# Kernel optimization log

Hardware: AMD Instinct MI355X
Metric: run time of the kernel (lower is better)

## Reference

```python
import jax, jax.numpy as jnp
import numpy as np

N = 100000          # nodes
E = 3200000         # edges (before self-loops)
F_IN = 500          # Pubmed feature dim
H1, C1 = 8, 8       # layer-1 heads, channels per head
H2, C2 = 1, 7       # layer-2 heads, channels (num classes)
NEG_SLOPE = 0.2


def _glorot(key, shape, fan_in):
    return jax.random.normal(key, shape, dtype=jnp.float32) / np.sqrt(fan_in)


def setup_inputs() -> dict:
    key = jax.random.key(0)
    ks = jax.random.split(key, 10)
    x = jax.random.normal(ks[0], (N, F_IN), dtype=jnp.float32)
    edge_index = jax.random.randint(ks[1], (2, E), 0, N, dtype=jnp.int64)
    W1 = _glorot(ks[2], (F_IN, H1 * C1), F_IN)
    a_src1 = _glorot(ks[3], (H1, C1), C1)
    a_dst1 = _glorot(ks[4], (H1, C1), C1)
    b1 = jnp.zeros((H1 * C1,), dtype=jnp.float32)
    W2 = _glorot(ks[5], (H1 * C1, H2 * C2), H1 * C1)
    a_src2 = _glorot(ks[6], (H2, C2), C2)
    a_dst2 = _glorot(ks[7], (H2, C2), C2)
    b2 = jnp.zeros((H2 * C2,), dtype=jnp.float32)
    return {"x": x, "edge_index": edge_index, "W1": W1, "a_src1": a_src1,
            "a_dst1": a_dst1, "b1": b1, "W2": W2, "a_src2": a_src2,
            "a_dst2": a_dst2, "b2": b2}


def gat_conv(x, src, dst, W, a_src, a_dst, bias, heads, out_ch):
    # x: [N, F_in]; src/dst: [E'] (self-loops included); returns [N, heads*out_ch]
    h = (x @ W).reshape(N, heads, out_ch)                      # [N, H, C]
    alpha_s = jnp.einsum('nhc,hc->nh', h, a_src)               # [N, H]
    alpha_d = jnp.einsum('nhc,hc->nh', h, a_dst)               # [N, H]
    e = alpha_s[src] + alpha_d[dst]                            # [E', H]
    e = jax.nn.leaky_relu(e, NEG_SLOPE)
    # segment softmax over incoming edges of each dst node
    m = jax.ops.segment_max(e, dst, num_segments=N)            # [N, H]
    ex = jnp.exp(e - m[dst])                                   # [E', H]
    denom = jax.ops.segment_sum(ex, dst, num_segments=N)       # [N, H]
    alpha = ex / denom[dst]                                    # [E', H]
    msg = alpha[:, :, None] * h[src]                           # [E', H, C]
    out = jax.ops.segment_sum(msg, dst, num_segments=N)        # [N, H, C]
    return out.reshape(N, heads * out_ch) + bias


def reference(x, edge_index, W1, a_src1, a_dst1, b1, W2, a_src2, a_dst2, b2):
    loops = jnp.arange(N, dtype=edge_index.dtype)
    src = jnp.concatenate([edge_index[0], loops])
    dst = jnp.concatenate([edge_index[1], loops])
    h = gat_conv(x, src, dst, W1, a_src1, a_dst1, b1, H1, C1)   # [N, 64]
    out = gat_conv(h, src, dst, W2, a_src2, a_dst2, b2, H2, C2) # [N, 7]
    return jax.nn.log_softmax(out, axis=1)
```

## Files before the change

### kernel.cpp

```cpp
#include <hip/hip_runtime.h>
#include <hip/hip_bf16.h>
#include <hip/hip_fp16.h>

#define N_NODES 100000
#define N_EDGES 3200000
#define ET (N_EDGES + N_NODES)
#define F_IN 500
#define H1 8
#define C1 8
#define F1 64
#define C2 7

#define BSH 6
#define NB ((N_NODES + 63) / 64)
#define CAP2 4096
#define FB 128
#define FCHUNK ((ET + FB - 1) / FB)

typedef __attribute__((ext_vector_type(8))) short short8;
typedef __attribute__((ext_vector_type(4))) float f32x4;

__device__ __forceinline__ unsigned short f2bf(float f) {
    const unsigned u = __float_as_uint(f);
    return (unsigned short)((u + 0x7FFFu + ((u >> 16) & 1u)) >> 16);
}

__global__ __launch_bounds__(1024) void fill_count(const int* __restrict__ ei,
                                                   int* __restrict__ cntmat) {
    __shared__ int hist[NB];
    const int t = threadIdx.x, blk = blockIdx.x;
    for (int i = t; i < NB; i += 1024) hist[i] = 0;
    __syncthreads();
    const int s0 = blk * FCHUNK;
    const int s1 = min(s0 + FCHUNK, ET);
    for (int i = s0 + t; i < s1; i += 1024) {
        const int dst = (i < N_EDGES) ? ei[N_EDGES + i] : (i - N_EDGES);
        atomicAdd(&hist[dst >> BSH], 1);
    }
    __syncthreads();
    int* row = cntmat + (size_t)blk * NB;
    for (int i = t; i < NB; i += 1024) row[i] = hist[i];
}

__global__ __launch_bounds__(1024) void scan2(const int* __restrict__ cntmat,
                                              int* __restrict__ boff,
                                              int* __restrict__ basemat) {
    __shared__ int tot[2048];
    __shared__ int wsum[16];
    const int t = threadIdx.x;
    const int lane = t & 63;
    const int w = t >> 6;
    for (int b = t; b < 2048; b += 1024) {
        int s = 0;
        if (b < NB)
            for (int j = 0; j < FB; ++j) s += cntmat[(size_t)j * NB + b];
        tot[b] = s;
    }
    __syncthreads();
    int running = 0;
    for (int t0 = 0; t0 < 2048; t0 += 1024) {
        const int v = tot[t0 + t];
        int sc = v;
#pragma unroll
        for (int d = 1; d < 64; d <<= 1) {
            int u = __shfl_up(sc, d);
            if (lane >= d) sc += u;
        }
        if (lane == 63) wsum[w] = sc;
        __syncthreads();
        if (t < 16) {
            int ws = wsum[t];
#pragma unroll
            for (int d = 1; d < 16; d <<= 1) {
                int u = __shfl_up(ws, d);
                if (t >= d) ws += u;
            }
            wsum[t] = ws;
        }
        __syncthreads();
        const int excl = running + (w ? wsum[w - 1] : 0) + sc - v;
        if (t0 + t < NB) boff[t0 + t] = excl;
        const int tt = wsum[15];
        __syncthreads();
        tot[t0 + t] = excl;
        running += tt;
    }
    if (t == 0) boff[NB] = running;
    __syncthreads();
    for (int b = t; b < NB; b += 1024) {
        int run = tot[b];
        for (int j = 0; j < FB; ++j) {
            basemat[(size_t)j * NB + b] = run;
            run += cntmat[(size_t)j * NB + b];
        }
    }
}

__global__ __launch_bounds__(1024) void fill_scatter(const int* __restrict__ ei,
                                                     const int* __restrict__ basemat,
                                                     unsigned int* __restrict__ ebuf) {
    __shared__ int cur[NB];
    const int t = threadIdx.x, blk = blockIdx.x;
    const int* row = basemat + (size_t)blk * NB;
    for (int i = t; i < NB; i += 1024) cur[i] = row[i];
    __syncthreads();
    const int s0 = blk * FCHUNK;
    const int s1 = min(s0 + FCHUNK, ET);
    for (int i = s0 + t; i < s1; i += 1024) {
        int src, dst;
        if (i < N_EDGES) { src = ei[i]; dst = ei[N_EDGES + i]; }
        else             { src = dst = i - N_EDGES; }
        const int b = dst >> BSH;
        const int p = atomicAdd(&cur[b], 1);
        ebuf[p] = (unsigned)src | ((unsigned)(dst & 63) << 17);
    }
}

__global__ __launch_bounds__(256) void wprep(const float* __restrict__ W1,
                                             short* __restrict__ wpk) {
    const int idx = blockIdx.x * 256 + threadIdx.x;
    if (idx >= 32768) return;
    const int j = idx & 7;
    const int l = (idx >> 3) & 63;
    const int f = (idx >> 9) & 3;
    const int ks = idx >> 11;
    const int k = ks * 32 + ((l >> 4) << 3) + j;
    const int col = f * 16 + (l & 15);
    const float fv = (k < F_IN) ? W1[k * F1 + col] : 0.f;
    wpk[idx] = (short)f2bf(fv);
}

__global__ __launch_bounds__(256) void gemm1_kernel(
    const float* __restrict__ x, const short* __restrict__ wpk,
    const float* __restrict__ a_src, const float* __restrict__ a_dst,
    __half* __restrict__ h1, float* __restrict__ as1, float* __restrict__ ad1)
{
    const int t = threadIdx.x;
    const int l = t & 63;
    const int w = t >> 6;
    const int row0 = blockIdx.x * 64 + w * 16;
    const int r = l & 15;
    const int koff = (l >> 4) * 8;
    const float* __restrict__ xp =
        x + (size_t)min(row0 + r, N_NODES - 1) * F_IN + koff;
    const short* __restrict__ wl = wpk + (l << 3);

    f32x4 acc[4];
#pragma unroll
    for (int f = 0; f < 4; ++f) acc[f] = (f32x4){0.f, 0.f, 0.f, 0.f};

    float4 va = *(const float4*)(xp);
    float4 vb = *(const float4*)(xp + 4);
    short8 bcur[4];
#pragma unroll
    for (int f = 0; f < 4; ++f)
        bcur[f] = *(const short8*)(wl + (f << 9));

    for (int ks = 0; ks < 16; ++ks) {
        float v[8];
        v[0] = va.x; v[1] = va.y; v[2] = va.z; v[3] = va.w;
        v[4] = vb.x; v[5] = vb.y; v[6] = vb.z; v[7] = vb.w;
        if (ks < 14) {
            va = *(const float4*)(xp + (ks + 1) * 32);
            vb = *(const float4*)(xp + (ks + 1) * 32 + 4);
        } else if (ks == 14) {
            float tv[8];
#pragma unroll
            for (int j = 0; j < 8; ++j)
                tv[j] = (koff + j < 20) ? xp[480 + j] : 0.f;
            va = make_float4(tv[0], tv[1], tv[2], tv[3]);
            vb = make_float4(tv[4], tv[5], tv[6], tv[7]);
        }
        short8 bnext[4];
        if (ks < 15) {
#pragma unroll
            for (int f = 0; f < 4; ++f)
                bnext[f] = *(const short8*)(wl + (((ks + 1) * 4 + f) << 9));
        }
        short8 ah, al;
#pragma unroll
        for (int j = 0; j < 8; ++j) {
            const unsigned short h = f2bf(v[j]);
            ah[j] = (short)h;
            al[j] = (short)f2bf(v[j] - __uint_as_float((unsigned)h << 16));
        }
#pragma unroll
        for (int f = 0; f < 4; ++f) {
            acc[f] = __builtin_amdgcn_mfma_f32_16x16x32_bf16(ah, bcur[f], acc[f], 0, 0, 0);
            acc[f] = __builtin_amdgcn_mfma_f32_16x16x32_bf16(al, bcur[f], acc[f], 0, 0, 0);
        }
        if (ks < 15) {
#pragma unroll
            for (int f = 0; f < 4; ++f) bcur[f] = bnext[f];
        }
    }

    const int g = l >> 4;
    const int p = r >> 3;
    float asv[4], adv[4];
#pragma unroll
    for (int f = 0; f < 4; ++f) {
        asv[f] = a_src[f * 16 + r];
        adv[f] = a_dst[f * 16 + r];
    }
#pragma unroll
    for (int f = 0; f < 4; ++f) {
#pragma unroll
        for (int reg = 0; reg < 4; ++reg) {
            const int row = row0 + g * 4 + reg;
            const float hv = acc[f][reg];
            if (row < N_NODES)
                h1[(size_t)row * F1 + f * 16 + r] = __float2half(hv);
            float ps = hv * asv[f];
            float pd = hv * adv[f];
            ps += __shfl_xor(ps, 1); ps += __shfl_xor(ps, 2); ps += __shfl_xor(ps, 4);
            pd += __shfl_xor(pd, 1); pd += __shfl_xor(pd, 2); pd += __shfl_xor(pd, 4);
            if ((l & 7) == 0 && row < N_NODES) {
                as1[row * H1 + f * 2 + p] = ps;
                ad1[row * H1 + f * 2 + p] = pd;
            }
        }
    }
}

__global__ __launch_bounds__(256) void agg1_kernel(
    const int* __restrict__ boff, const unsigned int* __restrict__ ebuf,
    const __half* __restrict__ h1, const float* __restrict__ as1,
    const float* __restrict__ ad1, const float* __restrict__ b1,
    float* __restrict__ hout)
{
    __shared__ int colb[CAP2];
    __shared__ int hist[64], curs[64], rowp[65];
    const int t = threadIdx.x, b = blockIdx.x;
    const int e0 = boff[b];
    const int cnt = boff[b + 1] - e0;
    const int l = t & 63;
    const int w = t >> 6;
    if (t < 64) hist[t] = 0;
    __syncthreads();

    if (cnt <= CAP2) {
        for (int i = t; i < cnt; i += 256)
            atomicAdd(&hist[ebuf[e0 + i] >> 17], 1);
        __syncthreads();
        if (t < 64) {
            const int v = hist[t];
            int sc = v;
#pragma unroll
            for (int d = 1; d < 64; d <<= 1) {
                int u = __shfl_up(sc, d);
                if (t >= d) sc += u;
            }
            rowp[t] = sc - v;
            curs[t] = sc - v;
            if (t == 63) rowp[64] = sc;
        }
        __syncthreads();
        for (int i = t; i < cnt; i += 256) {
            const unsigned v = ebuf[e0 + i];
            const int p = atomicAdd(&curs[v >> 17], 1);
            colb[p] = (int)(v & 0x1FFFFu);
        }
        __syncthreads();

        const int jsub = l & 7;
        const int hsub = l >> 3;
        const int pbase = l & 56;
        for (int ni = 0; ni < 16; ++ni) {
            const int d = w * 16 + ni;
            const int n = (b << 6) + d;
            if (n >= N_NODES) break;
            const int rr0 = rowp[d], rr1 = rowp[d + 1];
            const float adh = ad1[(n << 3) + hsub];
            float den = 0.f, acc = 0.f;
            int j0 = rr0;
            for (; j0 + 8 <= rr1; j0 += 8) {
                const int s_l = colb[j0 + jsub];
                float e = as1[(s_l << 3) + hsub] + adh;
                e = fmaxf(e, 0.2f * e);
                const float p_l = __expf(e);
#pragma unroll
                for (int j = 0; j < 8; ++j) {
                    const float p = __shfl(p_l, pbase + j);
                    const int s_j = __builtin_amdgcn_readlane(s_l, j);
                    const float v = __half2float(h1[((size_t)(unsigned)s_j << 6) + l]);
                    den += p;
                    acc = fmaf(p, v, acc);
                }
            }
            if (j0 < rr1) {
                const int s_l = colb[min(j0 + jsub, rr1 - 1)];
                float e = as1[(s_l << 3) + hsub] + adh;
                e = fmaxf(e, 0.2f * e);
                const float p_l = __expf(e);
#pragma unroll
                for (int j = 0; j < 8; ++j) {
                    if (j0 + j < rr1) {
                        const float p = __shfl(p_l, pbase + j);
                        const int s_j = __builtin_amdgcn_readlane(s_l, j);
                        const float v = __half2float(h1[((size_t)(unsigned)s_j << 6) + l]);
                        den += p;
                        acc = fmaf(p, v, acc);
                    }
                }
            }
            hout[((size_t)n << 6) + l] = acc / den + b1[l];
        }
    } else {
        const int hsub = l >> 3;
        for (int ni = 0; ni < 16; ++ni) {
            const int d = w * 16 + ni;
            const int n = (b << 6) + d;
            if (n >= N_NODES) break;
            const float adh = ad1[(n << 3) + hsub];
            float den = 0.f, acc = 0.f;
            for (int i = 0; i < cnt; ++i) {
                const unsigned v = ebuf[e0 + i];
                if ((int)(v >> 17) == d) {
                    const int s = (int)(v & 0x1FFFFu);
                    float e = as1[(s << 3) + hsub] + adh;
                    e = fmaxf(e, 0.2f * e);
                    const float p = __expf(e);
                    const float hv = __half2float(h1[((size_t)s << 6) + l]);
                    den += p;
                    acc = fmaf(p, hv, acc);
                }
            }
            hout[((size_t)n << 6) + l] = acc / den + b1[l];
        }
    }
}

__global__ __launch_bounds__(256) void gemm2_kernel(
    const float* __restrict__ hin, const float* __restrict__ W2,
    const float* __restrict__ a_src, const float* __restrict__ a_dst,
    float* __restrict__ h2p, float* __restrict__ as2, float* __restrict__ ad2)
{
    __shared__ float w2s[F1 * C2];
    __shared__ float as_s[C2], ad_s[C2];
    for (int i = threadIdx.x; i < F1 * C2; i += blockDim.x) w2s[i] = W2[i];
    if (threadIdx.x < C2) { as_s[threadIdx.x] = a_src[threadIdx.x]; ad_s[threadIdx.x] = a_dst[threadIdx.x]; }
    __syncthreads();

    int n = blockIdx.x * blockDim.x + threadIdx.x;
    if (n >= N_NODES) return;
    float acc[C2];
#pragma unroll
    for (int c = 0; c < C2; ++c) acc[c] = 0.f;
    const float* hp = hin + (size_t)n * F1;
    for (int k = 0; k < F1; k += 4) {
        const float4 hv = *(const float4*)(hp + k);
#pragma unroll
        for (int c = 0; c < C2; ++c) {
            acc[c] = fmaf(hv.x, w2s[(k + 0) * C2 + c], acc[c]);
            acc[c] = fmaf(hv.y, w2s[(k + 1) * C2 + c], acc[c]);
            acc[c] = fmaf(hv.z, w2s[(k + 2) * C2 + c], acc[c]);
            acc[c] = fmaf(hv.w, w2s[(k + 3) * C2 + c], acc[c]);
        }
    }
    float s = 0.f, d = 0.f;
#pragma unroll
    for (int c = 0; c < C2; ++c) {
        s = fmaf(acc[c], as_s[c], s);
        d = fmaf(acc[c], ad_s[c], d);
    }
    float4* o = (float4*)(h2p + (size_t)n * 8);
    o[0] = make_float4(acc[0], acc[1], acc[2], acc[3]);
    o[1] = make_float4(acc[4], acc[5], acc[6], 0.f);
    as2[n] = s;
    ad2[n] = d;
}

__global__ __launch_bounds__(256) void agg2_kernel(
    const int* __restrict__ boff, const unsigned int* __restrict__ ebuf,
    const float* __restrict__ h2p, const float* __restrict__ as2,
    const float* __restrict__ ad2, const float* __restrict__ b2,
    float* __restrict__ out)
{
    __shared__ int colb[CAP2];
    __shared__ int hist[64], curs[64], rowp[65];
    const int t = threadIdx.x, b = blockIdx.x;
    const int e0 = boff[b];
    const int cnt = boff[b + 1] - e0;
    if (t < 64) hist[t] = 0;
    __syncthreads();

    const int d = t >> 2;
    const int q = t & 3;
    const int n = (b << 6) + d;

    if (cnt <= CAP2) {
        for (int i = t; i < cnt; i += 256)
            atomicAdd(&hist[ebuf[e0 + i] >> 17], 1);
        __syncthreads();
        if (t < 64) {
            const int v = hist[t];
            int sc = v;
#pragma unroll
            for (int dd = 1; dd < 64; dd <<= 1) {
                int u = __shfl_up(sc, dd);
                if (t >= dd) sc += u;
            }
            rowp[t] = sc - v;
            curs[t] = sc - v;
            if (t == 63) rowp[64] = sc;
        }
        __syncthreads();
        for (int i = t; i < cnt; i += 256) {
            const unsigned v = ebuf[e0 + i];
            const int p = atomicAdd(&curs[v >> 17], 1);
            colb[p] = (int)(v & 0x1FFFFu);
        }
        __syncthreads();

        if (n >= N_NODES) return;
        const int rr0 = rowp[d], rr1 = rowp[d + 1];
        const float adn = ad2[n];
        float denom = 0.f;
        float a0 = 0, a1 = 0, a2 = 0, a3 = 0, a4 = 0, a5 = 0, a6 = 0;
        for (int j = rr0 + q; j < rr1; j += 4) {
            const int s = colb[j];
            float e = as2[s] + adn;
            e = fmaxf(e, 0.2f * e);
            const float ex = __expf(e);
            const float4 va = *(const float4*)(h2p + (size_t)s * 8);
            const float4 vb = *(const float4*)(h2p + (size_t)s * 8 + 4);
            denom += ex;
            a0 = fmaf(ex, va.x, a0); a1 = fmaf(ex, va.y, a1);
            a2 = fmaf(ex, va.z, a2); a3 = fmaf(ex, va.w, a3);
            a4 = fmaf(ex, vb.x, a4); a5 = fmaf(ex, vb.y, a5);
            a6 = fmaf(ex, vb.z, a6);
        }
#pragma unroll
        for (int dd = 1; dd < 4; dd <<= 1) {
            denom += __shfl_xor(denom, dd);
            a0 += __shfl_xor(a0, dd); a1 += __shfl_xor(a1, dd);
            a2 += __shfl_xor(a2, dd); a3 += __shfl_xor(a3, dd);
            a4 += __shfl_xor(a4, dd); a5 += __shfl_xor(a5, dd);
            a6 += __shfl_xor(a6, dd);
        }
        const float inv = 1.f / denom;
        float v0 = a0 * inv + b2[0], v1 = a1 * inv + b2[1];
        float v2 = a2 * inv + b2[2], v3 = a3 * inv + b2[3];
        float v4 = a4 * inv + b2[4], v5 = a5 * inv + b2[5];
        float v6 = a6 * inv + b2[6];
        float mx = fmaxf(fmaxf(fmaxf(v0, v1), fmaxf(v2, v3)), fmaxf(fmaxf(v4, v5), v6));
        const float se = __expf(v0 - mx) + __expf(v1 - mx) + __expf(v2 - mx) +
                         __expf(v3 - mx) + __expf(v4 - mx) + __expf(v5 - mx) +
                         __expf(v6 - mx);
        const float lse = __logf(se) + mx;
        const float wa = (q == 0) ? v0 : (q == 1) ? v1 : (q == 2) ? v2 : v3;
        const float wb = (q == 0) ? v4 : (q == 1) ? v5 : v6;
        out[n * C2 + q] = wa - lse;
        if (q < 3) out[n * C2 + q + 4] = wb - lse;
    } else {
        if (n >= N_NODES) return;
        const float adn = ad2[n];
        float denom = 0.f;
        float a0 = 0, a1 = 0, a2 = 0, a3 = 0, a4 = 0, a5 = 0, a6 = 0;
        for (int i = q; i < cnt; i += 4) {
            const unsigned v = ebuf[e0 + i];
            if ((int)(v >> 17) == d) {
                const int s = (int)(v & 0x1FFFFu);
                float e = as2[s] + adn;
                e = fmaxf(e, 0.2f * e);
                const float ex = __expf(e);
                const float4 va = *(const float4*)(h2p + (size_t)s * 8);
                const float4 vb = *(const float4*)(h2p + (size_t)s * 8 + 4);
                denom += ex;
                a0 = fmaf(ex, va.x, a0); a1 = fmaf(ex, va.y, a1);
                a2 = fmaf(ex, va.z, a2); a3 = fmaf(ex, va.w, a3);
                a4 = fmaf(ex, vb.x, a4); a5 = fmaf(ex, vb.y, a5);
                a6 = fmaf(ex, vb.z, a6);
            }
        }
#pragma unroll
        for (int dd = 1; dd < 4; dd <<= 1) {
            denom += __shfl_xor(denom, dd);
            a0 += __shfl_xor(a0, dd); a1 += __shfl_xor(a1, dd);
            a2 += __shfl_xor(a2, dd); a3 += __shfl_xor(a3, dd);
            a4 += __shfl_xor(a4, dd); a5 += __shfl_xor(a5, dd);
            a6 += __shfl_xor(a6, dd);
        }
        const float inv = 1.f / denom;
        float v0 = a0 * inv + b2[0], v1 = a1 * inv + b2[1];
        float v2 = a2 * inv + b2[2], v3 = a3 * inv + b2[3];
        float v4 = a4 * inv + b2[4], v5 = a5 * inv + b2[5];
        float v6 = a6 * inv + b2[6];
        float mx = fmaxf(fmaxf(fmaxf(v0, v1), fmaxf(v2, v3)), fmaxf(fmaxf(v4, v5), v6));
        const float se = __expf(v0 - mx) + __expf(v1 - mx) + __expf(v2 - mx) +
                         __expf(v3 - mx) + __expf(v4 - mx) + __expf(v5 - mx) +
                         __expf(v6 - mx);
        const float lse = __logf(se) + mx;
        const float wa = (q == 0) ? v0 : (q == 1) ? v1 : (q == 2) ? v2 : v3;
        const float wb = (q == 0) ? v4 : (q == 1) ? v5 : v6;
        out[n * C2 + q] = wa - lse;
        if (q < 3) out[n * C2 + q + 4] = wb - lse;
    }
}

extern "C" void kernel_launch(void* const* d_in, const int* in_sizes, int n_in,
                              void* d_out, int out_size, void* d_ws, size_t ws_size,
                              hipStream_t stream) {
    const float* x      = (const float*)d_in[0];
    const int*   ei     = (const int*)  d_in[1];
    const float* W1     = (const float*)d_in[2];
    const float* a_src1 = (const float*)d_in[3];
    const float* a_dst1 = (const float*)d_in[4];
    const float* b1     = (const float*)d_in[5];
    const float* W2     = (const float*)d_in[6];
    const float* a_src2 = (const float*)d_in[7];
    const float* a_dst2 = (const float*)d_in[8];
    const float* b2     = (const float*)d_in[9];
    float* out = (float*)d_out;

    char* ws = (char*)d_ws;
    size_t off = 0;
    auto alloc = [&](size_t bytes) -> void* {
        void* p = ws + off;
        off += (bytes + 255) & ~(size_t)255;
        return p;
    };
    int*          boff    = (int*)   alloc((size_t)(NB + 1) * sizeof(int));
    int*          cntmat  = (int*)   alloc((size_t)FB * NB * sizeof(int));
    int*          basemat = (int*)   alloc((size_t)FB * NB * sizeof(int));
    unsigned int* ebuf    = (unsigned int*)alloc((size_t)ET * sizeof(unsigned int));
    short*        wpk     = (short*) alloc((size_t)32768 * sizeof(short));
    __half*       h1      = (__half*)alloc((size_t)N_NODES * F1 * sizeof(__half));
    float*        as1     = (float*) alloc((size_t)N_NODES * H1 * sizeof(float));
    float*        ad1     = (float*) alloc((size_t)N_NODES * H1 * sizeof(float));
    float*        hout1   = (float*) alloc((size_t)N_NODES * F1 * sizeof(float));
    float*        h2p     = (float*) alloc((size_t)N_NODES * 8 * sizeof(float));
    float*        as2     = (float*) alloc((size_t)N_NODES * sizeof(float));
    float*        ad2     = (float*) alloc((size_t)N_NODES * sizeof(float));

    wprep<<<128, 256, 0, stream>>>(W1, wpk);
    fill_count<<<FB, 1024, 0, stream>>>(ei, cntmat);
    scan2<<<1, 1024, 0, stream>>>(cntmat, boff, basemat);
    fill_scatter<<<FB, 1024, 0, stream>>>(ei, basemat, ebuf);
    gemm1_kernel<<<(N_NODES + 63) / 64, 256, 0, stream>>>(x, wpk, a_src1, a_dst1, h1, as1, ad1);
    agg1_kernel<<<NB, 256, 0, stream>>>(boff, ebuf, h1, as1, ad1, b1, hout1);
    gemm2_kernel<<<(N_NODES + 255) / 256, 256, 0, stream>>>(hout1, W2, a_src2, a_dst2, h2p, as2, ad2);
    agg2_kernel<<<NB, 256, 0, stream>>>(boff, ebuf, h2p, as2, ad2, b2, out);
}
```

Baseline: 336.5 us.

## Fuse layer-2 projection into agg1, parallelize scan, double-buffer gemm1 loads

Three separate changes. The per-bucket prefix over the FB block rows moves out of the single-block scan into its own multi-block kernel, so that serial work is spread across many blocks. The gemm1 x-row loads are double-buffered two k-steps ahead with the loop fully unrolled to hide global latency. The 64x7 layer-2 projection and its attention logits are fused into agg1 through wave-wide shuffle reductions, which removes the 25.6 MB hout1 write/read and one kernel launch at the cost of 42 shuffles per node and extra registers in agg1.

```diff
diff --git a/kernel.cpp b/kernel.cpp
--- a/kernel.cpp
+++ b/kernel.cpp
@@ -42,9 +42,9 @@
     for (int i = t; i < NB; i += 1024) row[i] = hist[i];
 }
 
-__global__ __launch_bounds__(1024) void scan2(const int* __restrict__ cntmat,
-                                              int* __restrict__ boff,
-                                              int* __restrict__ basemat) {
+__global__ __launch_bounds__(1024) void scan2a(const int* __restrict__ cntmat,
+                                               int* __restrict__ boff,
+                                               int* __restrict__ bexcl) {
     __shared__ int tot[2048];
     __shared__ int wsum[16];
     const int t = threadIdx.x;
@@ -79,20 +79,27 @@
         }
         __syncthreads();
         const int excl = running + (w ? wsum[w - 1] : 0) + sc - v;
-        if (t0 + t < NB) boff[t0 + t] = excl;
+        if (t0 + t < NB) {
+            boff[t0 + t] = excl;
+            bexcl[t0 + t] = excl;
+        }
         const int tt = wsum[15];
         __syncthreads();
-        tot[t0 + t] = excl;
         running += tt;
     }
     if (t == 0) boff[NB] = running;
-    __syncthreads();
-    for (int b = t; b < NB; b += 1024) {
-        int run = tot[b];
-        for (int j = 0; j < FB; ++j) {
-            basemat[(size_t)j * NB + b] = run;
-            run += cntmat[(size_t)j * NB + b];
-        }
+}
+
+__global__ __launch_bounds__(256) void scan2b(const int* __restrict__ cntmat,
+                                              const int* __restrict__ bexcl,
+                                              int* __restrict__ basemat) {
+    const int b = blockIdx.x * 256 + threadIdx.x;
+    if (b >= NB) return;
+    int run = bexcl[b];
+#pragma unroll 4
+    for (int j = 0; j < FB; ++j) {
+        basemat[(size_t)j * NB + b] = run;
+        run += cntmat[(size_t)j * NB + b];
     }
 }
 
@@ -149,27 +156,30 @@
 #pragma unroll
     for (int f = 0; f < 4; ++f) acc[f] = (f32x4){0.f, 0.f, 0.f, 0.f};
 
-    float4 va = *(const float4*)(xp);
-    float4 vb = *(const float4*)(xp + 4);
+    float4 va[2], vb[2];
+    va[0] = *(const float4*)(xp);       vb[0] = *(const float4*)(xp + 4);
+    va[1] = *(const float4*)(xp + 32);  vb[1] = *(const float4*)(xp + 36);
     short8 bcur[4];
 #pragma unroll
     for (int f = 0; f < 4; ++f)
         bcur[f] = *(const short8*)(wl + (f << 9));
 
+#pragma unroll
     for (int ks = 0; ks < 16; ++ks) {
+        const int s = ks & 1;
         float v[8];
-        v[0] = va.x; v[1] = va.y; v[2] = va.z; v[3] = va.w;
-        v[4] = vb.x; v[5] = vb.y; v[6] = vb.z; v[7] = vb.w;
-        if (ks < 14) {
-            va = *(const float4*)(xp + (ks + 1) * 32);
-            vb = *(const float4*)(xp + (ks + 1) * 32 + 4);
-        } else if (ks == 14) {
+        v[0] = va[s].x; v[1] = va[s].y; v[2] = va[s].z; v[3] = va[s].w;
+        v[4] = vb[s].x; v[5] = vb[s].y; v[6] = vb[s].z; v[7] = vb[s].w;
+        if (ks + 2 < 15) {
+            va[s] = *(const float4*)(xp + (ks + 2) * 32);
+            vb[s] = *(const float4*)(xp + (ks + 2) * 32 + 4);
+        } else if (ks + 2 == 15) {
             float tv[8];
 #pragma unroll
             for (int j = 0; j < 8; ++j)
                 tv[j] = (koff + j < 20) ? xp[480 + j] : 0.f;
-            va = make_float4(tv[0], tv[1], tv[2], tv[3]);
-            vb = make_float4(tv[4], tv[5], tv[6], tv[7]);
+            va[s] = make_float4(tv[0], tv[1], tv[2], tv[3]);
+            vb[s] = make_float4(tv[4], tv[5], tv[6], tv[7]);
         }
         short8 bnext[4];
         if (ks < 15) {
@@ -227,7 +237,9 @@
     const int* __restrict__ boff, const unsigned int* __restrict__ ebuf,
     const __half* __restrict__ h1, const float* __restrict__ as1,
     const float* __restrict__ ad1, const float* __restrict__ b1,
-    float* __restrict__ hout)
+    const float* __restrict__ W2, const float* __restrict__ as2c,
+    const float* __restrict__ ad2c,
+    float* __restrict__ h2p, float* __restrict__ as2, float* __restrict__ ad2)
 {
     __shared__ int colb[CAP2];
     __shared__ int hist[64], curs[64], rowp[65];
@@ -239,7 +251,17 @@
     if (t < 64) hist[t] = 0;
     __syncthreads();
 
-    if (cnt <= CAP2) {
+    float w2row[C2], asc2[C2], adc2[C2];
+#pragma unroll
+    for (int c = 0; c < C2; ++c) {
+        w2row[c] = W2[l * C2 + c];
+        asc2[c] = as2c[c];
+        adc2[c] = ad2c[c];
+    }
+    const float b1l = b1[l];
+
+    const bool sorted = (cnt <= CAP2);
+    if (sorted) {
         for (int i = t; i < cnt; i += 256)
             atomicAdd(&hist[ebuf[e0 + i] >> 17], 1);
         __syncthreads();
@@ -262,17 +284,19 @@
             colb[p] = (int)(v & 0x1FFFFu);
         }
         __syncthreads();
-
-        const int jsub = l & 7;
-        const int hsub = l >> 3;
-        const int pbase = l & 56;
-        for (int ni = 0; ni < 16; ++ni) {
-            const int d = w * 16 + ni;
-            const int n = (b << 6) + d;
-            if (n >= N_NODES) break;
+    }
+
+    const int jsub = l & 7;
+    const int hsub = l >> 3;
+    const int pbase = l & 56;
+    for (int ni = 0; ni < 16; ++ni) {
+        const int d = w * 16 + ni;
+        const int n = (b << 6) + d;
+        if (n >= N_NODES) break;
+        const float adh = ad1[(n << 3) + hsub];
+        float den = 0.f, accv = 0.f;
+        if (sorted) {
             const int rr0 = rowp[d], rr1 = rowp[d + 1];
-            const float adh = ad1[(n << 3) + hsub];
-            float den = 0.f, acc = 0.f;
             int j0 = rr0;
             for (; j0 + 8 <= rr1; j0 += 8) {
                 const int s_l = colb[j0 + jsub];
@@ -285,7 +309,7 @@
                     const int s_j = __builtin_amdgcn_readlane(s_l, j);
                     const float v = __half2float(h1[((size_t)(unsigned)s_j << 6) + l]);
                     den += p;
-                    acc = fmaf(p, v, acc);
+                    accv = fmaf(p, v, accv);
                 }
             }
             if (j0 < rr1) {
@@ -300,20 +324,11 @@
                         const int s_j = __builtin_amdgcn_readlane(s_l, j);
                         const float v = __half2float(h1[((size_t)(unsigned)s_j << 6) + l]);
                         den += p;
-                        acc = fmaf(p, v, acc);
+                        accv = fmaf(p, v, accv);
                     }
                 }
             }
-            hout[((size_t)n << 6) + l] = acc / den + b1[l];
-        }
-    } else {
-        const int hsub = l >> 3;
-        for (int ni = 0; ni < 16; ++ni) {
-            const int d = w * 16 + ni;
-            const int n = (b << 6) + d;
-            if (n >= N_NODES) break;
-            const float adh = ad1[(n << 3) + hsub];
-            float den = 0.f, acc = 0.f;
+        } else {
             for (int i = 0; i < cnt; ++i) {
                 const unsigned v = ebuf[e0 + i];
                 if ((int)(v >> 17) == d) {
@@ -321,54 +336,37 @@
                     float e = as1[(s << 3) + hsub] + adh;
                     e = fmaxf(e, 0.2f * e);
                     const float p = __expf(e);
-                    const float hv = __half2float(h1[((size_t)s << 6) + l]);
+                    const float hv0 = __half2float(h1[((size_t)s << 6) + l]);
                     den += p;
-                    acc = fmaf(p, hv, acc);
+                    accv = fmaf(p, hv0, accv);
                 }
             }
-            hout[((size_t)n << 6) + l] = acc / den + b1[l];
-        }
-    }
-}
-
-__global__ __launch_bounds__(256) void gemm2_kernel(
-    const float* __restrict__ hin, const float* __restrict__ W2,
-    const float* __restrict__ a_src, const float* __restrict__ a_dst,
-    float* __restrict__ h2p, float* __restrict__ as2, float* __restrict__ ad2)
-{
-    __shared__ float w2s[F1 * C2];
-    __shared__ float as_s[C2], ad_s[C2];
-    for (int i = threadIdx.x; i < F1 * C2; i += blockDim.x) w2s[i] = W2[i];
-    if (threadIdx.x < C2) { as_s[threadIdx.x] = a_src[threadIdx.x]; ad_s[threadIdx.x] = a_dst[threadIdx.x]; }
-    __syncthreads();
-
-    int n = blockIdx.x * blockDim.x + threadIdx.x;
-    if (n >= N_NODES) return;
-    float acc[C2];
-#pragma unroll
-    for (int c = 0; c < C2; ++c) acc[c] = 0.f;
-    const float* hp = hin + (size_t)n * F1;
-    for (int k = 0; k < F1; k += 4) {
-        const float4 hv = *(const float4*)(hp + k);
-#pragma unroll
-        for (int c = 0; c < C2; ++c) {
-            acc[c] = fmaf(hv.x, w2s[(k + 0) * C2 + c], acc[c]);
-            acc[c] = fmaf(hv.y, w2s[(k + 1) * C2 + c], acc[c]);
-            acc[c] = fmaf(hv.z, w2s[(k + 2) * C2 + c], acc[c]);
-            acc[c] = fmaf(hv.w, w2s[(k + 3) * C2 + c], acc[c]);
-        }
-    }
-    float s = 0.f, d = 0.f;
-#pragma unroll
-    for (int c = 0; c < C2; ++c) {
-        s = fmaf(acc[c], as_s[c], s);
-        d = fmaf(acc[c], ad_s[c], d);
-    }
-    float4* o = (float4*)(h2p + (size_t)n * 8);
-    o[0] = make_float4(acc[0], acc[1], acc[2], acc[3]);
-    o[1] = make_float4(acc[4], acc[5], acc[6], 0.f);
-    as2[n] = s;
-    ad2[n] = d;
+        }
+        const float hv = accv / den + b1l;
+
+        float prod[C2];
+#pragma unroll
+        for (int c = 0; c < C2; ++c) prod[c] = hv * w2row[c];
+#pragma unroll
+        for (int dd = 1; dd < 64; dd <<= 1) {
+#pragma unroll
+            for (int c = 0; c < C2; ++c) prod[c] += __shfl_xor(prod[c], dd);
+        }
+        if (l == 0) {
+            *(float4*)(h2p + ((size_t)n << 3)) =
+                make_float4(prod[0], prod[1], prod[2], prod[3]);
+            *(float4*)(h2p + ((size_t)n << 3) + 4) =
+                make_float4(prod[4], prod[5], prod[6], 0.f);
+            float sv = 0.f, dv = 0.f;
+#pragma unroll
+            for (int c = 0; c < C2; ++c) {
+                sv = fmaf(prod[c], asc2[c], sv);
+                dv = fmaf(prod[c], adc2[c], dv);
+            }
+            as2[n] = sv;
+            ad2[n] = dv;
+        }
+    }
 }
 
 __global__ __launch_bounds__(256) void agg2_kernel(
@@ -522,6 +520,7 @@
         return p;
     };
     int*          boff    = (int*)   alloc((size_t)(NB + 1) * sizeof(int));
+    int*          bexcl   = (int*)   alloc((size_t)NB * sizeof(int));
     int*          cntmat  = (int*)   alloc((size_t)FB * NB * sizeof(int));
     int*          basemat = (int*)   alloc((size_t)FB * NB * sizeof(int));
     unsigned int* ebuf    = (unsigned int*)alloc((size_t)ET * sizeof(unsigned int));
@@ -529,17 +528,17 @@
     __half*       h1      = (__half*)alloc((size_t)N_NODES * F1 * sizeof(__half));
     float*        as1     = (float*) alloc((size_t)N_NODES * H1 * sizeof(float));
     float*        ad1     = (float*) alloc((size_t)N_NODES * H1 * sizeof(float));
-    float*        hout1   = (float*) alloc((size_t)N_NODES * F1 * sizeof(float));
     float*        h2p     = (float*) alloc((size_t)N_NODES * 8 * sizeof(float));
     float*        as2     = (float*) alloc((size_t)N_NODES * sizeof(float));
     float*        ad2     = (float*) alloc((size_t)N_NODES * sizeof(float));
 
     wprep<<<128, 256, 0, stream>>>(W1, wpk);
     fill_count<<<FB, 1024, 0, stream>>>(ei, cntmat);
-    scan2<<<1, 1024, 0, stream>>>(cntmat, boff, basemat);
+    scan2a<<<1, 1024, 0, stream>>>(cntmat, boff, bexcl);
+    scan2b<<<(NB + 255) / 256, 256, 0, stream>>>(cntmat, bexcl, basemat);
     fill_scatter<<<FB, 1024, 0, stream>>>(ei, basemat, ebuf);
     gemm1_kernel<<<(N_NODES + 63) / 64, 256, 0, stream>>>(x, wpk, a_src1, a_dst1, h1, as1, ad1);
-    agg1_kernel<<<NB, 256, 0, stream>>>(boff, ebuf, h1, as1, ad1, b1, hout1);
-    gemm2_kernel<<<(N_NODES + 255) / 256, 256, 0, stream>>>(hout1, W2, a_src2, a_dst2, h2p, as2, ad2);
+    agg1_kernel<<<NB, 256, 0, stream>>>(boff, ebuf, h1, as1, ad1, b1,
+                                        W2, a_src2, a_dst2, h2p, as2, ad2);
     agg2_kernel<<<NB, 256, 0, stream>>>(boff, ebuf, h2p, as2, ad2, b2, out);
 }
```

Measured after the change: 344.4 us. 2.4% more time.

## Split scan, cache per-block CSR from agg1, store layer-1 output as fp16

Applied to the files above, without the earlier changes.

The single-block scan's serial per-bucket prefix loop moves into a separate multi-block kernel (scan2b), so that work is spread across many blocks. agg1 now writes its locally sorted column indices and row pointers to global memory, and agg2 reads them instead of redoing the histogram/sort in shared memory. The layer-1 output hout1 is stored as fp16, halving its write and read traffic into gemm2. The costs are one extra launch, an extra global write of about 3.3M column indices, and reduced precision on the hidden activations.

```diff
diff --git a/kernel.cpp b/kernel.cpp
--- a/kernel.cpp
+++ b/kernel.cpp
@@ -42,9 +42,9 @@
     for (int i = t; i < NB; i += 1024) row[i] = hist[i];
 }
 
-__global__ __launch_bounds__(1024) void scan2(const int* __restrict__ cntmat,
-                                              int* __restrict__ boff,
-                                              int* __restrict__ basemat) {
+__global__ __launch_bounds__(1024) void scan2a(const int* __restrict__ cntmat,
+                                               int* __restrict__ boff,
+                                               int* __restrict__ bexcl) {
     __shared__ int tot[2048];
     __shared__ int wsum[16];
     const int t = threadIdx.x;
@@ -79,20 +79,27 @@
         }
         __syncthreads();
         const int excl = running + (w ? wsum[w - 1] : 0) + sc - v;
-        if (t0 + t < NB) boff[t0 + t] = excl;
+        if (t0 + t < NB) {
+            boff[t0 + t] = excl;
+            bexcl[t0 + t] = excl;
+        }
         const int tt = wsum[15];
         __syncthreads();
-        tot[t0 + t] = excl;
         running += tt;
     }
     if (t == 0) boff[NB] = running;
-    __syncthreads();
-    for (int b = t; b < NB; b += 1024) {
-        int run = tot[b];
-        for (int j = 0; j < FB; ++j) {
-            basemat[(size_t)j * NB + b] = run;
-            run += cntmat[(size_t)j * NB + b];
-        }
+}
+
+__global__ __launch_bounds__(256) void scan2b(const int* __restrict__ cntmat,
+                                              const int* __restrict__ bexcl,
+                                              int* __restrict__ basemat) {
+    const int b = blockIdx.x * 256 + threadIdx.x;
+    if (b >= NB) return;
+    int run = bexcl[b];
+#pragma unroll 4
+    for (int j = 0; j < FB; ++j) {
+        basemat[(size_t)j * NB + b] = run;
+        run += cntmat[(size_t)j * NB + b];
     }
 }
 
@@ -227,7 +234,8 @@
     const int* __restrict__ boff, const unsigned int* __restrict__ ebuf,
     const __half* __restrict__ h1, const float* __restrict__ as1,
     const float* __restrict__ ad1, const float* __restrict__ b1,
-    float* __restrict__ hout)
+    __half* __restrict__ hout, int* __restrict__ colidx,
+    int* __restrict__ rowptrg)
 {
     __shared__ int colb[CAP2];
     __shared__ int hist[64], curs[64], rowp[65];
@@ -262,6 +270,8 @@
             colb[p] = (int)(v & 0x1FFFFu);
         }
         __syncthreads();
+        for (int i = t; i < cnt; i += 256) colidx[e0 + i] = colb[i];
+        if (t < 65) rowptrg[b * 65 + t] = e0 + rowp[t];
 
         const int jsub = l & 7;
         const int hsub = l >> 3;
@@ -304,7 +314,7 @@
                     }
                 }
             }
-            hout[((size_t)n << 6) + l] = acc / den + b1[l];
+            hout[((size_t)n << 6) + l] = __float2half(acc / den + b1[l]);
         }
     } else {
         const int hsub = l >> 3;
@@ -326,13 +336,13 @@
                     acc = fmaf(p, hv, acc);
                 }
             }
-            hout[((size_t)n << 6) + l] = acc / den + b1[l];
+            hout[((size_t)n << 6) + l] = __float2half(acc / den + b1[l]);
         }
     }
 }
 
 __global__ __launch_bounds__(256) void gemm2_kernel(
-    const float* __restrict__ hin, const float* __restrict__ W2,
+    const __half* __restrict__ hin, const float* __restrict__ W2,
     const float* __restrict__ a_src, const float* __restrict__ a_dst,
     float* __restrict__ h2p, float* __restrict__ as2, float* __restrict__ ad2)
 {
@@ -347,15 +357,17 @@
     float acc[C2];
 #pragma unroll
     for (int c = 0; c < C2; ++c) acc[c] = 0.f;
-    const float* hp = hin + (size_t)n * F1;
-    for (int k = 0; k < F1; k += 4) {
-        const float4 hv = *(const float4*)(hp + k);
-#pragma unroll
-        for (int c = 0; c < C2; ++c) {
-            acc[c] = fmaf(hv.x, w2s[(k + 0) * C2 + c], acc[c]);
-            acc[c] = fmaf(hv.y, w2s[(k + 1) * C2 + c], acc[c]);
-            acc[c] = fmaf(hv.z, w2s[(k + 2) * C2 + c], acc[c]);
-            acc[c] = fmaf(hv.w, w2s[(k + 3) * C2 + c], acc[c]);
+    const short8* hp = (const short8*)(hin + ((size_t)n << 6));
+#pragma unroll
+    for (int k8 = 0; k8 < 8; ++k8) {
+        const short8 h8 = hp[k8];
+#pragma unroll
+        for (int e = 0; e < 8; ++e) {
+            const float hv = __half2float(__ushort_as_half((unsigned short)h8[e]));
+            const int k = k8 * 8 + e;
+#pragma unroll
+            for (int c = 0; c < C2; ++c)
+                acc[c] = fmaf(hv, w2s[k * C2 + c], acc[c]);
         }
     }
     float s = 0.f, d = 0.f;
@@ -373,53 +385,25 @@
 
 __global__ __launch_bounds__(256) void agg2_kernel(
     const int* __restrict__ boff, const unsigned int* __restrict__ ebuf,
+    const int* __restrict__ rowptrg, const int* __restrict__ colidx,
     const float* __restrict__ h2p, const float* __restrict__ as2,
     const float* __restrict__ ad2, const float* __restrict__ b2,
     float* __restrict__ out)
 {
-    __shared__ int colb[CAP2];
-    __shared__ int hist[64], curs[64], rowp[65];
     const int t = threadIdx.x, b = blockIdx.x;
-    const int e0 = boff[b];
-    const int cnt = boff[b + 1] - e0;
-    if (t < 64) hist[t] = 0;
-    __syncthreads();
-
     const int d = t >> 2;
     const int q = t & 3;
     const int n = (b << 6) + d;
-
+    if (n >= N_NODES) return;
+    const int cnt = boff[b + 1] - boff[b];
+    const float adn = ad2[n];
+
+    float denom = 0.f;
+    float a0 = 0, a1 = 0, a2 = 0, a3 = 0, a4 = 0, a5 = 0, a6 = 0;
     if (cnt <= CAP2) {
-        for (int i = t; i < cnt; i += 256)
-            atomicAdd(&hist[ebuf[e0 + i] >> 17], 1);
-        __syncthreads();
-        if (t < 64) {
-            const int v = hist[t];
-            int sc = v;
-#pragma unroll
-            for (int dd = 1; dd < 64; dd <<= 1) {
-                int u = __shfl_up(sc, dd);
-                if (t >= dd) sc += u;
-            }
-            rowp[t] = sc - v;
-            curs[t] = sc - v;
-            if (t == 63) rowp[64] = sc;
-        }
-        __syncthreads();
-        for (int i = t; i < cnt; i += 256) {
-            const unsigned v = ebuf[e0 + i];
-            const int p = atomicAdd(&curs[v >> 17], 1);
-            colb[p] = (int)(v & 0x1FFFFu);
-        }
-        __syncthreads();
-
-        if (n >= N_NODES) return;
-        const int rr0 = rowp[d], rr1 = rowp[d + 1];
-        const float adn = ad2[n];
-        float denom = 0.f;
-        float a0 = 0, a1 = 0, a2 = 0, a3 = 0, a4 = 0, a5 = 0, a6 = 0;
+        const int rr0 = rowptrg[b * 65 + d], rr1 = rowptrg[b * 65 + d + 1];
         for (int j = rr0 + q; j < rr1; j += 4) {
-            const int s = colb[j];
+            const int s = colidx[j];
             float e = as2[s] + adn;
             e = fmaxf(e, 0.2f * e);
             const float ex = __expf(e);
@@ -431,33 +415,8 @@
             a4 = fmaf(ex, vb.x, a4); a5 = fmaf(ex, vb.y, a5);
             a6 = fmaf(ex, vb.z, a6);
         }
-#pragma unroll
-        for (int dd = 1; dd < 4; dd <<= 1) {
-            denom += __shfl_xor(denom, dd);
-            a0 += __shfl_xor(a0, dd); a1 += __shfl_xor(a1, dd);
-            a2 += __shfl_xor(a2, dd); a3 += __shfl_xor(a3, dd);
-            a4 += __shfl_xor(a4, dd); a5 += __shfl_xor(a5, dd);
-            a6 += __shfl_xor(a6, dd);
-        }
-        const float inv = 1.f / denom;
-        float v0 = a0 * inv + b2[0], v1 = a1 * inv + b2[1];
-        float v2 = a2 * inv + b2[2], v3 = a3 * inv + b2[3];
-        float v4 = a4 * inv + b2[4], v5 = a5 * inv + b2[5];
-        float v6 = a6 * inv + b2[6];
-        float mx = fmaxf(fmaxf(fmaxf(v0, v1), fmaxf(v2, v3)), fmaxf(fmaxf(v4, v5), v6));
-        const float se = __expf(v0 - mx) + __expf(v1 - mx) + __expf(v2 - mx) +
-                         __expf(v3 - mx) + __expf(v4 - mx) + __expf(v5 - mx) +
-                         __expf(v6 - mx);
-        const float lse = __logf(se) + mx;
-        const float wa = (q == 0) ? v0 : (q == 1) ? v1 : (q == 2) ? v2 : v3;
-        const float wb = (q == 0) ? v4 : (q == 1) ? v5 : v6;
-        out[n * C2 + q] = wa - lse;
-        if (q < 3) out[n * C2 + q + 4] = wb - lse;
     } else {
-        if (n >= N_NODES) return;
-        const float adn = ad2[n];
-        float denom = 0.f;
-        float a0 = 0, a1 = 0, a2 = 0, a3 = 0, a4 = 0, a5 = 0, a6 = 0;
+        const int e0 = boff[b];
         for (int i = q; i < cnt; i += 4) {
             const unsigned v = ebuf[e0 + i];
             if ((int)(v >> 17) == d) {
@@ -474,29 +433,29 @@
                 a6 = fmaf(ex, vb.z, a6);
             }
         }
-#pragma unroll
-        for (int dd = 1; dd < 4; dd <<= 1) {
-            denom += __shfl_xor(denom, dd);
-            a0 += __shfl_xor(a0, dd); a1 += __shfl_xor(a1, dd);
-            a2 += __shfl_xor(a2, dd); a3 += __shfl_xor(a3, dd);
-            a4 += __shfl_xor(a4, dd); a5 += __shfl_xor(a5, dd);
-            a6 += __shfl_xor(a6, dd);
-        }
-        const float inv = 1.f / denom;
-        float v0 = a0 * inv + b2[0], v1 = a1 * inv + b2[1];
-        float v2 = a2 * inv + b2[2], v3 = a3 * inv + b2[3];
-        float v4 = a4 * inv + b2[4], v5 = a5 * inv + b2[5];
-        float v6 = a6 * inv + b2[6];
-        float mx = fmaxf(fmaxf(fmaxf(v0, v1), fmaxf(v2, v3)), fmaxf(fmaxf(v4, v5), v6));
-        const float se = __expf(v0 - mx) + __expf(v1 - mx) + __expf(v2 - mx) +
-                         __expf(v3 - mx) + __expf(v4 - mx) + __expf(v5 - mx) +
-                         __expf(v6 - mx);
-        const float lse = __logf(se) + mx;
-        const float wa = (q == 0) ? v0 : (q == 1) ? v1 : (q == 2) ? v2 : v3;
-        const float wb = (q == 0) ? v4 : (q == 1) ? v5 : v6;
-        out[n * C2 + q] = wa - lse;
-        if (q < 3) out[n * C2 + q + 4] = wb - lse;
-    }
+    }
+#pragma unroll
+    for (int dd = 1; dd < 4; dd <<= 1) {
+        denom += __shfl_xor(denom, dd);
+        a0 += __shfl_xor(a0, dd); a1 += __shfl_xor(a1, dd);
+        a2 += __shfl_xor(a2, dd); a3 += __shfl_xor(a3, dd);
+        a4 += __shfl_xor(a4, dd); a5 += __shfl_xor(a5, dd);
+        a6 += __shfl_xor(a6, dd);
+    }
+    const float inv = 1.f / denom;
+    float v0 = a0 * inv + b2[0], v1 = a1 * inv + b2[1];
+    float v2 = a2 * inv + b2[2], v3 = a3 * inv + b2[3];
+    float v4 = a4 * inv + b2[4], v5 = a5 * inv + b2[5];
+    float v6 = a6 * inv + b2[6];
+    float mx = fmaxf(fmaxf(fmaxf(v0, v1), fmaxf(v2, v3)), fmaxf(fmaxf(v4, v5), v6));
+    const float se = __expf(v0 - mx) + __expf(v1 - mx) + __expf(v2 - mx) +
+                     __expf(v3 - mx) + __expf(v4 - mx) + __expf(v5 - mx) +
+                     __expf(v6 - mx);
+    const float lse = __logf(se) + mx;
+    const float wa = (q == 0) ? v0 : (q == 1) ? v1 : (q == 2) ? v2 : v3;
+    const float wb = (q == 0) ? v4 : (q == 1) ? v5 : v6;
+    out[n * C2 + q] = wa - lse;
+    if (q < 3) out[n * C2 + q + 4] = wb - lse;
 }
 
 extern "C" void kernel_launch(void* const* d_in, const int* in_sizes, int n_in,
@@ -522,24 +481,28 @@
         return p;
     };
     int*          boff    = (int*)   alloc((size_t)(NB + 1) * sizeof(int));
+    int*          bexcl   = (int*)   alloc((size_t)NB * sizeof(int));
     int*          cntmat  = (int*)   alloc((size_t)FB * NB * sizeof(int));
     int*          basemat = (int*)   alloc((size_t)FB * NB * sizeof(int));
     unsigned int* ebuf    = (unsigned int*)alloc((size_t)ET * sizeof(unsigned int));
+    int*          colidx  = (int*)   alloc((size_t)ET * sizeof(int));
+    int*          rowptrg = (int*)   alloc((size_t)NB * 65 * sizeof(int));
     short*        wpk     = (short*) alloc((size_t)32768 * sizeof(short));
     __half*       h1      = (__half*)alloc((size_t)N_NODES * F1 * sizeof(__half));
     float*        as1     = (float*) alloc((size_t)N_NODES * H1 * sizeof(float));
     float*        ad1     = (float*) alloc((size_t)N_NODES * H1 * sizeof(float));
-    float*        hout1   = (float*) alloc((size_t)N_NODES * F1 * sizeof(float));
+    __half*       hout1   = (__half*)alloc((size_t)N_NODES * F1 * sizeof(__half));
     float*        h2p     = (float*) alloc((size_t)N_NODES * 8 * sizeof(float));
     float*        as2     = (float*) alloc((size_t)N_NODES * sizeof(float));
     float*        ad2     = (float*) alloc((size_t)N_NODES * sizeof(float));
 
     wprep<<<128, 256, 0, stream>>>(W1, wpk);
     fill_count<<<FB, 1024, 0, stream>>>(ei, cntmat);
-    scan2<<<1, 1024, 0, stream>>>(cntmat, boff, basemat);
+    scan2a<<<1, 1024, 0, stream>>>(cntmat, boff, bexcl);
+    scan2b<<<(NB + 255) / 256, 256, 0, stream>>>(cntmat, bexcl, basemat);
     fill_scatter<<<FB, 1024, 0, stream>>>(ei, basemat, ebuf);
     gemm1_kernel<<<(N_NODES + 63) / 64, 256, 0, stream>>>(x, wpk, a_src1, a_dst1, h1, as1, ad1);
-    agg1_kernel<<<NB, 256, 0, stream>>>(boff, ebuf, h1, as1, ad1, b1, hout1);
+    agg1_kernel<<<NB, 256, 0, stream>>>(boff, ebuf, h1, as1, ad1, b1, hout1, colidx, rowptrg);
     gemm2_kernel<<<(N_NODES + 255) / 256, 256, 0, stream>>>(hout1, W2, a_src2, a_dst2, h2p, as2, ad2);
-    agg2_kernel<<<NB, 256, 0, stream>>>(boff, ebuf, h2p, as2, ad2, b2, out);
-}
+    agg2_kernel<<<NB, 256, 0, stream>>>(boff, ebuf, rowptrg, colidx, h2p, as2, ad2, b2, out);
+}
```

New measurement: 345.9 us. 1.03x slower.
